# Kernel optimization log

Hardware: AMD Instinct MI355X
Metric: run time of the kernel (lower is better)

Reference implementation:

```python
import jax, jax.numpy as jnp
import numpy as np

B, N, C, H = 2, 2048, 512, 8
D = C // H  # head dim = 64
SCALE = C ** -0.5  # module uses heads_channels**-0.5 (full inner dim, not per-head)


def setup_inputs() -> dict:
    key = jax.random.key(0)
    ks = jax.random.split(key, 9)
    return {
        "q": jax.random.normal(ks[0], (B, N, C), jnp.float32),
        "kv": jax.random.normal(ks[1], (B, N, C), jnp.float32),
        "pos_q": jax.random.normal(ks[2], (B, N, D), jnp.float32),
        "pos_k": jax.random.normal(ks[3], (B, N, D), jnp.float32),
        "Wq": jax.random.normal(ks[4], (C, C), jnp.float32) * (C ** -0.5),
        "Wk": jax.random.normal(ks[5], (C, C), jnp.float32) * (C ** -0.5),
        "Wv": jax.random.normal(ks[6], (C, C), jnp.float32) * (C ** -0.5),
        "Wo": jax.random.normal(ks[7], (C, C), jnp.float32) * (C ** -0.5),
        "bo": jnp.zeros((C,), jnp.float32),
    }


def reference(q, kv, pos_q, pos_k, Wq, Wk, Wv, Wo, bo):
    # projections: [b n c] @ [c c] -> [b n c]
    qp = q @ Wq
    kp = kv @ Wk
    vp = kv @ Wv
    # split heads: b n (h d) -> b h n d
    split = lambda t: t.reshape(B, N, H, D).transpose(0, 2, 1, 3)
    qh, kh, vh = split(qp), split(kp), split(vp)
    # additive positional bias, broadcast over heads: b n d -> b 1 n d
    qh = qh + pos_q[:, None, :, :]
    kh = kh + pos_k[:, None, :, :]
    sim = jnp.einsum("bhid,bhjd->bhij", qh, kh) * SCALE
    attn = jax.nn.softmax(sim, axis=-1)
    out = jnp.einsum("bhij,bhjd->bhid", attn, vh)
    # merge heads: b h n d -> b n (h d)
    out = out.transpose(0, 2, 1, 3).reshape(B, N, C)
    return out @ Wo + bo
```

## Files before the change

### kernel.cpp

```cpp
#include <hip/hip_runtime.h>
#include <hip/hip_bf16.h>
#include <stdint.h>
#include <math.h>

static constexpr int kB = 2, kN = 2048, kC = 512, kH = 8, kD = 64;
static constexpr float kScaleL2E =
    (float)(0.044194173824159216 * 1.4426950408889634);
static constexpr int kSplit = 2;
static constexpr size_t kSegF = (size_t)kB * kN * kC;

typedef short bf16x8 __attribute__((ext_vector_type(8)));
typedef short bf16x4 __attribute__((ext_vector_type(4)));
typedef float f32x4  __attribute__((ext_vector_type(4)));

__device__ __forceinline__ float bf2f(unsigned short u) {
  union { unsigned int i; float f; } v; v.i = ((unsigned int)u) << 16; return v.f;
}
__device__ __forceinline__ unsigned short f2bf(float f) {
  union { float f; unsigned int i; } v; v.f = f;
  unsigned int x = v.i;
  return (unsigned short)((x + 0x7FFFu + ((x >> 16) & 1u)) >> 16);
}
__device__ __forceinline__ short f2bs(float f) { return (short)f2bf(f); }
__device__ __forceinline__ unsigned int pack2_t(float lo, float hi) {
  union { float f; unsigned int i; } a, b; a.f = lo; b.f = hi;
  return (b.i & 0xFFFF0000u) | (a.i >> 16);
}
__device__ __forceinline__ float fast_exp2(float x) {
#if __has_builtin(__builtin_amdgcn_exp2f)
  return __builtin_amdgcn_exp2f(x);
#else
  return exp2f(x);
#endif
}

__device__ __forceinline__ int vcol(int k) {
  return 32 * (k >> 5) + ((k >> 2) & 3) * 8 + ((k >> 4) & 1) * 4;
}

__global__ __launch_bounds__(256) void prep_kernel(
    const float* __restrict__ q, const float* __restrict__ kv,
    const float* __restrict__ Wq, const float* __restrict__ Wk,
    const float* __restrict__ Wv,
    unsigned short* __restrict__ qbf, unsigned short* __restrict__ kvbf,
    unsigned short* __restrict__ wT)
{
  const int t = threadIdx.x;
  if (blockIdx.z == 0) {
    const int gid = blockIdx.x * 256 + t;
    #pragma unroll
    for (int it = 0; it < 8; ++it) {
      int i4 = gid + it * 65536;
      float4 a = *(const float4*)(q + (size_t)i4 * 4);
      float4 b = *(const float4*)(kv + (size_t)i4 * 4);
      bf16x4 ab = {f2bs(a.x), f2bs(a.y), f2bs(a.z), f2bs(a.w)};
      bf16x4 bb = {f2bs(b.x), f2bs(b.y), f2bs(b.z), f2bs(b.w)};
      *(bf16x4*)(qbf + (size_t)i4 * 4) = ab;
      *(bf16x4*)(kvbf + (size_t)i4 * 4) = bb;
    }
  } else {
    if (blockIdx.x >= 192) return;
    const int wsel = blockIdx.x >> 6;
    const int tile = blockIdx.x & 63;
    const int tr = tile >> 3, tc = tile & 7;
    const float* W = (wsel == 0) ? Wq : (wsel == 1 ? Wk : Wv);
    unsigned short* out = wT + (size_t)wsel * kC * kC;

    __shared__ __align__(16) float Ts[64][68];
    #pragma unroll
    for (int it = 0; it < 4; ++it) {
      int e = t + it * 256;
      int r = e >> 4, c4 = (e & 15) * 4;
      *(float4*)&Ts[r][c4] =
          *(const float4*)(W + (size_t)(tr * 64 + r) * kC + tc * 64 + c4);
    }
    __syncthreads();
    const int n = t >> 2, ks = (t & 3) * 16;
    unsigned short* orow = out + (size_t)(tc * 64 + n) * kC + tr * 64 + ks;
    #pragma unroll
    for (int c = 0; c < 4; ++c) {
      ushort4 o;
      o.x = f2bf(Ts[ks + c * 4 + 0][n]);
      o.y = f2bf(Ts[ks + c * 4 + 1][n]);
      o.z = f2bf(Ts[ks + c * 4 + 2][n]);
      o.w = f2bf(Ts[ks + c * 4 + 3][n]);
      *(ushort4*)(orow + c * 4) = o;
    }
  }
}

__global__ __launch_bounds__(256) void proj_kernel(
    const unsigned short* __restrict__ qbf,
    const unsigned short* __restrict__ kvbf,
    const unsigned short* __restrict__ wT,
    const float* __restrict__ pos_q,
    const float* __restrict__ pos_k,
    unsigned short* __restrict__ qh,
    unsigned short* __restrict__ kh,
    unsigned short* __restrict__ vhT)
{
  const bool kvmode = (blockIdx.z == 1);
  const unsigned short* A = kvmode ? kvbf : qbf;
  const unsigned short* Bt0 = wT + (kvmode ? (size_t)kC * kC : 0);
  const unsigned short* Bt1 = wT + 2 * (size_t)kC * kC;

  __shared__ __align__(16) unsigned short As[2][128][72];
  __shared__ __align__(16) unsigned short Bs[2][2][64][72];

  const int t = threadIdx.x;
  const int w = t >> 6, lane = t & 63;
  const int l15 = lane & 15, quad = lane >> 4;
  const int m0 = blockIdx.x * 128;
  const int n0 = blockIdx.y * 64;

  const int sr = t >> 3, sc = (t & 7) * 8;

  bf16x8 pa[4], pb0[2], pb1[2];
  #pragma unroll
  for (int i = 0; i < 4; ++i)
    pa[i] = *(const bf16x8*)(A + (size_t)(m0 + sr + i * 32) * kC + sc);
  #pragma unroll
  for (int i = 0; i < 2; ++i)
    pb0[i] = *(const bf16x8*)(Bt0 + (size_t)(n0 + sr + i * 32) * kC + sc);
  if (kvmode)
    #pragma unroll
    for (int i = 0; i < 2; ++i)
      pb1[i] = *(const bf16x8*)(Bt1 + (size_t)(n0 + sr + i * 32) * kC + sc);

  #pragma unroll
  for (int i = 0; i < 4; ++i) *(bf16x8*)&As[0][sr + i * 32][sc] = pa[i];
  #pragma unroll
  for (int i = 0; i < 2; ++i) *(bf16x8*)&Bs[0][0][sr + i * 32][sc] = pb0[i];
  if (kvmode)
    #pragma unroll
    for (int i = 0; i < 2; ++i) *(bf16x8*)&Bs[0][1][sr + i * 32][sc] = pb1[i];

  #pragma unroll
  for (int i = 0; i < 4; ++i)
    pa[i] = *(const bf16x8*)(A + (size_t)(m0 + sr + i * 32) * kC + 64 + sc);
  #pragma unroll
  for (int i = 0; i < 2; ++i)
    pb0[i] = *(const bf16x8*)(Bt0 + (size_t)(n0 + sr + i * 32) * kC + 64 + sc);
  if (kvmode)
    #pragma unroll
    for (int i = 0; i < 2; ++i)
      pb1[i] = *(const bf16x8*)(Bt1 + (size_t)(n0 + sr + i * 32) * kC + 64 + sc);

  f32x4 acc0[2][4], acc1[2][4];
  #pragma unroll
  for (int si = 0; si < 2; ++si)
    #pragma unroll
    for (int ct = 0; ct < 4; ++ct) {
      acc0[si][ct] = (f32x4){0.f, 0.f, 0.f, 0.f};
      acc1[si][ct] = (f32x4){0.f, 0.f, 0.f, 0.f};
    }

  const int nkt = kC / 64;
  for (int it = 0; it < nkt; ++it) {
    __syncthreads();
    if (it + 1 < nkt) {
      const int wb = (it + 1) & 1;
      #pragma unroll
      for (int i = 0; i < 4; ++i) *(bf16x8*)&As[wb][sr + i * 32][sc] = pa[i];
      #pragma unroll
      for (int i = 0; i < 2; ++i) *(bf16x8*)&Bs[wb][0][sr + i * 32][sc] = pb0[i];
      if (kvmode)
        #pragma unroll
        for (int i = 0; i < 2; ++i) *(bf16x8*)&Bs[wb][1][sr + i * 32][sc] = pb1[i];
      if (it + 2 < nkt) {
        const int kn = (it + 2) * 64;
        #pragma unroll
        for (int i = 0; i < 4; ++i)
          pa[i] = *(const bf16x8*)(A + (size_t)(m0 + sr + i * 32) * kC + kn + sc);
        #pragma unroll
        for (int i = 0; i < 2; ++i)
          pb0[i] = *(const bf16x8*)(Bt0 + (size_t)(n0 + sr + i * 32) * kC + kn + sc);
        if (kvmode)
          #pragma unroll
          for (int i = 0; i < 2; ++i)
            pb1[i] = *(const bf16x8*)(Bt1 + (size_t)(n0 + sr + i * 32) * kC + kn + sc);
      }
    }
    const int ib = it & 1;
    bf16x8 a0[2], a1[2];
    #pragma unroll
    for (int si = 0; si < 2; ++si) {
      a0[si] = *(const bf16x8*)&As[ib][w * 32 + si * 16 + l15][quad * 8];
      a1[si] = *(const bf16x8*)&As[ib][w * 32 + si * 16 + l15][32 + quad * 8];
    }
    #pragma unroll
    for (int ct = 0; ct < 4; ++ct) {
      bf16x8 b0 = *(const bf16x8*)&Bs[ib][0][ct * 16 + l15][quad * 8];
      bf16x8 b1 = *(const bf16x8*)&Bs[ib][0][ct * 16 + l15][32 + quad * 8];
      #pragma unroll
      for (int si = 0; si < 2; ++si) {
        acc0[si][ct] = __builtin_amdgcn_mfma_f32_16x16x32_bf16(a0[si], b0, acc0[si][ct], 0, 0, 0);
        acc0[si][ct] = __builtin_amdgcn_mfma_f32_16x16x32_bf16(a1[si], b1, acc0[si][ct], 0, 0, 0);
      }
      if (kvmode) {
        bf16x8 c0 = *(const bf16x8*)&Bs[ib][1][ct * 16 + l15][quad * 8];
        bf16x8 c1 = *(const bf16x8*)&Bs[ib][1][ct * 16 + l15][32 + quad * 8];
        #pragma unroll
        for (int si = 0; si < 2; ++si) {
          acc1[si][ct] = __builtin_amdgcn_mfma_f32_16x16x32_bf16(a0[si], c0, acc1[si][ct], 0, 0, 0);
          acc1[si][ct] = __builtin_amdgcn_mfma_f32_16x16x32_bf16(a1[si], c1, acc1[si][ct], 0, 0, 0);
        }
      }
    }
  }

  const int h = n0 >> 6;
  if (!kvmode) {
    #pragma unroll
    for (int si = 0; si < 2; ++si)
      #pragma unroll
      for (int r = 0; r < 4; ++r) {
        int m = m0 + w * 32 + si * 16 + quad * 4 + r;
        int b = m >> 11, n_seq = m & (kN - 1);
        #pragma unroll
        for (int ct = 0; ct < 4; ++ct) {
          int d = ct * 16 + l15;
          float val = (acc0[si][ct][r] +
                       pos_q[((size_t)b * kN + n_seq) * kD + d]) * kScaleL2E;
          qh[(((size_t)b * kH + h) * kN + n_seq) * kD + d] = f2bf(val);
        }
      }
  } else {
    #pragma unroll
    for (int si = 0; si < 2; ++si)
      #pragma unroll
      for (int r = 0; r < 4; ++r) {
        int m = m0 + w * 32 + si * 16 + quad * 4 + r;
        int b = m >> 11, n_seq = m & (kN - 1);
        #pragma unroll
        for (int ct = 0; ct < 4; ++ct) {
          int d = ct * 16 + l15;
          float vk = acc0[si][ct][r] + pos_k[((size_t)b * kN + n_seq) * kD + d];
          kh[(((size_t)b * kH + h) * kN + n_seq) * kD + d] = f2bf(vk);
        }
      }
    __syncthreads();
    unsigned short (*Tv)[136] = (unsigned short(*)[136])&As[0][0][0];
    #pragma unroll
    for (int si = 0; si < 2; ++si)
      #pragma unroll
      for (int ct = 0; ct < 4; ++ct) {
        const int d = ct * 16 + l15;
        const int nl = w * 32 + si * 16 + quad * 4;
        unsigned int lo = (unsigned int)f2bf(acc1[si][ct][0]) |
                          ((unsigned int)f2bf(acc1[si][ct][1]) << 16);
        unsigned int hi = (unsigned int)f2bf(acc1[si][ct][2]) |
                          ((unsigned int)f2bf(acc1[si][ct][3]) << 16);
        *(unsigned int*)&Tv[d][nl]     = lo;
        *(unsigned int*)&Tv[d][nl + 2] = hi;
      }
    __syncthreads();
    const int c16 = t & 15, dr = t >> 4;
    const int b2 = m0 >> 11, nbase = m0 & (kN - 1);
    #pragma unroll
    for (int rep = 0; rep < 4; ++rep) {
      const int d = rep * 16 + dr;
      bf16x8 vv = *(const bf16x8*)&Tv[d][c16 * 8];
      *(bf16x8*)(vhT + (((size_t)(b2 * kH + h)) * kD + d) * kN + nbase + c16 * 8) = vv;
    }
  }
}

__global__ __launch_bounds__(256, 8) void attn_kernel(
    const unsigned short* __restrict__ qh,
    const unsigned short* __restrict__ kh,
    const unsigned short* __restrict__ vhT,
    unsigned short* __restrict__ opart,
    float* __restrict__ lbuf)
{
  const int sid = (blockIdx.x & 7) * 128 + (blockIdx.x >> 3);
  const int s  = sid >> 9;
  const int bh = (sid >> 5) & 15;
  const int q0 = (sid & 31) * 64;
  const int b = bh >> 3, h = bh & 7;
  const int kbase = s * (kN / kSplit);
  const int nkt = kN / kSplit / 64;
  const int t = threadIdx.x;
  const int w = t >> 6, lane = t & 63;
  const int l15 = lane & 15, quad = lane >> 4;

  __shared__ __align__(16) unsigned short Kb_s[2][64][72];
  __shared__ __align__(16) unsigned short Vt_s[2][64][72];

  const unsigned short* Qb = qh  + (size_t)bh * kN * kD;
  const unsigned short* Kb = kh  + (size_t)bh * kN * kD;
  const unsigned short* Vb = vhT + (size_t)bh * kD * kN;

  bf16x8 aq0, aq1;
  {
    const unsigned short* qrow = Qb + (size_t)(q0 + w * 16 + l15) * kD;
    aq0 = *(const bf16x8*)(qrow + quad * 8);
    aq1 = *(const bf16x8*)(qrow + 32 + quad * 8);
  }

  const int sr = t >> 3, sc = (t & 7) * 8, sr2 = sr + 32;
  const int vc1 = vcol(sc), vc2 = vcol(sc + 4);

  const unsigned short* pK0 = Kb + (size_t)(kbase + sr) * kD + sc;
  const unsigned short* pK1 = Kb + (size_t)(kbase + sr2) * kD + sc;
  const unsigned short* pV0 = Vb + (size_t)sr * kN + kbase + sc;
  const unsigned short* pV1 = Vb + (size_t)sr2 * kN + kbase + sc;
  const size_t kStepK = (size_t)64 * kD;

  {
    bf16x8 k0v = *(const bf16x8*)pK0;
    bf16x8 k1v = *(const bf16x8*)pK1;
    bf16x8 v0v = *(const bf16x8*)pV0;
    bf16x8 v1v = *(const bf16x8*)pV1;
    *(bf16x8*)&Kb_s[0][sr][sc]  = k0v;
    *(bf16x8*)&Kb_s[0][sr2][sc] = k1v;
    bf16x4 lo0 = {v0v[0], v0v[1], v0v[2], v0v[3]};
    bf16x4 hi0 = {v0v[4], v0v[5], v0v[6], v0v[7]};
    bf16x4 lo1 = {v1v[0], v1v[1], v1v[2], v1v[3]};
    bf16x4 hi1 = {v1v[4], v1v[5], v1v[6], v1v[7]};
    *(bf16x4*)&Vt_s[0][sr][vc1]  = lo0;
    *(bf16x4*)&Vt_s[0][sr][vc2]  = hi0;
    *(bf16x4*)&Vt_s[0][sr2][vc1] = lo1;
    *(bf16x4*)&Vt_s[0][sr2][vc2] = hi1;
  }
  pK0 += kStepK; pK1 += kStepK; pV0 += 64; pV1 += 64;
  bf16x8 pk0 = *(const bf16x8*)pK0;
  bf16x8 pk1 = *(const bf16x8*)pK1;
  bf16x8 pv0 = *(const bf16x8*)pV0;
  bf16x8 pv1 = *(const bf16x8*)pV1;

  f32x4 o[4];
  #pragma unroll
  for (int nt = 0; nt < 4; ++nt) o[nt] = (f32x4){0.f, 0.f, 0.f, 0.f};
  float l_run = 0.f;

  for (int i = 0; i < nkt; ++i) {
    __syncthreads();
    const unsigned short (*Kr)[72] = Kb_s[i & 1];
    const unsigned short (*Vr)[72] = Vt_s[i & 1];

    f32x4 sacc[4];
    __builtin_amdgcn_s_setprio(1);
    #pragma unroll
    for (int ct = 0; ct < 4; ++ct) {
      bf16x8 ak0 = *(const bf16x8*)&Kr[ct * 16 + l15][quad * 8];
      bf16x8 ak1 = *(const bf16x8*)&Kr[ct * 16 + l15][32 + quad * 8];
      f32x4 zz = (f32x4){0.f, 0.f, 0.f, 0.f};
      zz = __builtin_amdgcn_mfma_f32_16x16x32_bf16(ak0, aq0, zz, 0, 0, 0);
      zz = __builtin_amdgcn_mfma_f32_16x16x32_bf16(ak1, aq1, zz, 0, 0, 0);
      sacc[ct] = zz;
    }
    __builtin_amdgcn_s_setprio(0);

    union PB8 { unsigned int u[4]; bf16x8 v; } pb01, pb23;
    {
      float psum = 0.f;
      #pragma unroll
      for (int ct = 0; ct < 4; ++ct)
        #pragma unroll
        for (int r = 0; r < 4; ++r) {
          float p = fast_exp2(sacc[ct][r]);
          sacc[ct][r] = p;
          psum += p;
        }
      l_run += psum;
      pb01.u[0] = pack2_t(sacc[0][0], sacc[0][1]);
      pb01.u[1] = pack2_t(sacc[0][2], sacc[0][3]);
      pb01.u[2] = pack2_t(sacc[1][0], sacc[1][1]);
      pb01.u[3] = pack2_t(sacc[1][2], sacc[1][3]);
      pb23.u[0] = pack2_t(sacc[2][0], sacc[2][1]);
      pb23.u[1] = pack2_t(sacc[2][2], sacc[2][3]);
      pb23.u[2] = pack2_t(sacc[3][0], sacc[3][1]);
      pb23.u[3] = pack2_t(sacc[3][2], sacc[3][3]);
    }

    __builtin_amdgcn_s_setprio(1);
    #pragma unroll
    for (int nt = 0; nt < 4; ++nt) {
      bf16x8 av0 = *(const bf16x8*)&Vr[nt * 16 + l15][quad * 8];
      bf16x8 av1 = *(const bf16x8*)&Vr[nt * 16 + l15][32 + quad * 8];
      o[nt] = __builtin_amdgcn_mfma_f32_16x16x32_bf16(av0, pb01.v, o[nt], 0, 0, 0);
      o[nt] = __builtin_amdgcn_mfma_f32_16x16x32_bf16(av1, pb23.v, o[nt], 0, 0, 0);
    }
    __builtin_amdgcn_s_setprio(0);

    if (i + 1 < nkt) {
      unsigned short (*Kw)[72] = Kb_s[(i + 1) & 1];
      unsigned short (*Vw)[72] = Vt_s[(i + 1) & 1];
      *(bf16x8*)&Kw[sr][sc]  = pk0;
      *(bf16x8*)&Kw[sr2][sc] = pk1;
      bf16x4 lo0 = {pv0[0], pv0[1], pv0[2], pv0[3]};
      bf16x4 hi0 = {pv0[4], pv0[5], pv0[6], pv0[7]};
      bf16x4 lo1 = {pv1[0], pv1[1], pv1[2], pv1[3]};
      bf16x4 hi1 = {pv1[4], pv1[5], pv1[6], pv1[7]};
      *(bf16x4*)&Vw[sr][vc1]  = lo0;
      *(bf16x4*)&Vw[sr][vc2]  = hi0;
      *(bf16x4*)&Vw[sr2][vc1] = lo1;
      *(bf16x4*)&Vw[sr2][vc2] = hi1;
      if (i + 2 < nkt) {
        pK0 += kStepK; pK1 += kStepK; pV0 += 64; pV1 += 64;
        pk0 = *(const bf16x8*)pK0;
        pk1 = *(const bf16x8*)pK1;
        pv0 = *(const bf16x8*)pV0;
        pv1 = *(const bf16x8*)pV1;
      }
    }
  }

  l_run += __shfl_xor(l_run, 16);
  l_run += __shfl_xor(l_run, 32);
  if (quad == 0)
    lbuf[(size_t)(s * 16 + bh) * kN + q0 + w * 16 + l15] = l_run;

  __syncthreads();
  unsigned short (*Ot)[72] = (unsigned short(*)[72])&Kb_s[0][0][0];
  {
    const int ql = w * 16 + l15;
    #pragma unroll
    for (int nt = 0; nt < 4; ++nt) {
      unsigned int lo = (unsigned int)f2bf(o[nt][0]) |
                        ((unsigned int)f2bf(o[nt][1]) << 16);
      unsigned int hi = (unsigned int)f2bf(o[nt][2]) |
                        ((unsigned int)f2bf(o[nt][3]) << 16);
      const int d0 = nt * 16 + quad * 4;
      *(unsigned int*)&Ot[ql][d0]     = lo;
      *(unsigned int*)&Ot[ql][d0 + 2] = hi;
    }
  }
  __syncthreads();
  {
    unsigned short* od = opart + (size_t)s * kSegF;
    const int c8 = t & 7, qb = t >> 3;
    #pragma unroll
    for (int rep = 0; rep < 2; ++rep) {
      const int ql = rep * 32 + qb;
      bf16x8 vv = *(const bf16x8*)&Ot[ql][c8 * 8];
      *(bf16x8*)(od + ((size_t)b * kN + (q0 + ql)) * kC + h * kD + c8 * 8) = vv;
    }
  }
}

__global__ __launch_bounds__(256) void proj_out_kernel(
    const unsigned short* __restrict__ opart,
    const float* __restrict__ lbuf,
    const float* __restrict__ Wo,
    const float* __restrict__ bo,
    float* __restrict__ out)
{
  __shared__ __align__(16) unsigned short Wt[2][64][72];

  const int t = threadIdx.x;
  const int w = t >> 6, lane = t & 63;
  const int l15 = lane & 15, quad = lane >> 4;
  const int m0 = blockIdx.x * 64;
  const int n0 = blockIdx.y * 64;

  const int m = m0 + w * 16 + l15;
  const int nseq = m & (kN - 1);
  const int bb = m >> 11;
  const size_t arow = (size_t)m * kC;

  ushort4 pw[4];
  #pragma unroll
  for (int i = 0; i < 4; ++i) {
    int e = t + i * 256;
    int r = e >> 4, c4 = (e & 15) * 4;
    float4 wv = *(const float4*)(Wo + (size_t)r * kC + n0 + c4);
    pw[i] = make_ushort4(f2bf(wv.x), f2bf(wv.y), f2bf(wv.z), f2bf(wv.w));
  }
  #pragma unroll
  for (int i = 0; i < 4; ++i) {
    int e = t + i * 256;
    int r = e >> 4, c4 = (e & 15) * 4;
    Wt[0][c4 + 0][r] = pw[i].x;
    Wt[0][c4 + 1][r] = pw[i].y;
    Wt[0][c4 + 2][r] = pw[i].z;
    Wt[0][c4 + 3][r] = pw[i].w;
  }
  #pragma unroll
  for (int i = 0; i < 4; ++i) {
    int e = t + i * 256;
    int r = e >> 4, c4 = (e & 15) * 4;
    float4 wv = *(const float4*)(Wo + (size_t)(64 + r) * kC + n0 + c4);
    pw[i] = make_ushort4(f2bf(wv.x), f2bf(wv.y), f2bf(wv.z), f2bf(wv.w));
  }

  f32x4 acc[4];
  #pragma unroll
  for (int ct = 0; ct < 4; ++ct) acc[ct] = (f32x4){0.f, 0.f, 0.f, 0.f};

  const int nkt = kC / 64;
  for (int it = 0; it < nkt; ++it) {
    const int k0 = it * 64;
    __syncthreads();
    if (it + 1 < nkt) {
      const int wb = (it + 1) & 1;
      #pragma unroll
      for (int i = 0; i < 4; ++i) {
        int e = t + i * 256;
        int r = e >> 4, c4 = (e & 15) * 4;
        Wt[wb][c4 + 0][r] = pw[i].x;
        Wt[wb][c4 + 1][r] = pw[i].y;
        Wt[wb][c4 + 2][r] = pw[i].z;
        Wt[wb][c4 + 3][r] = pw[i].w;
      }
      if (it + 2 < nkt) {
        const int kn = (it + 2) * 64;
        #pragma unroll
        for (int i = 0; i < 4; ++i) {
          int e = t + i * 256;
          int r = e >> 4, c4 = (e & 15) * 4;
          float4 wv = *(const float4*)(Wo + (size_t)(kn + r) * kC + n0 + c4);
          pw[i] = make_ushort4(f2bf(wv.x), f2bf(wv.y), f2bf(wv.z), f2bf(wv.w));
        }
      }
    }

    const int h = k0 >> 6;
    const int bh = bb * 8 + h;
    float lsum = 0.f;
    #pragma unroll
    for (int s = 0; s < kSplit; ++s)
      lsum += lbuf[(size_t)(s * 16 + bh) * kN + nseq];
    const float wgt = 1.f / lsum;

    float af0[8] = {}, af1[8] = {};
    #pragma unroll
    for (int s = 0; s < kSplit; ++s) {
      bf16x8 v0 = *(const bf16x8*)(opart + (size_t)s * kSegF + arow + k0 + quad * 8);
      bf16x8 v1 = *(const bf16x8*)(opart + (size_t)s * kSegF + arow + k0 + 32 + quad * 8);
      #pragma unroll
      for (int j = 0; j < 8; ++j) {
        af0[j] += bf2f((unsigned short)v0[j]);
        af1[j] += bf2f((unsigned short)v1[j]);
      }
    }
    bf16x8 a0, a1;
    #pragma unroll
    for (int j = 0; j < 8; ++j) {
      a0[j] = (short)f2bf(af0[j] * wgt);
      a1[j] = (short)f2bf(af1[j] * wgt);
    }

    const int ib = it & 1;
    #pragma unroll
    for (int ct = 0; ct < 4; ++ct) {
      bf16x8 b0 = *(const bf16x8*)&Wt[ib][ct * 16 + l15][quad * 8];
      bf16x8 b1 = *(const bf16x8*)&Wt[ib][ct * 16 + l15][32 + quad * 8];
      acc[ct] = __builtin_amdgcn_mfma_f32_16x16x32_bf16(a0, b0, acc[ct], 0, 0, 0);
      acc[ct] = __builtin_amdgcn_mfma_f32_16x16x32_bf16(a1, b1, acc[ct], 0, 0, 0);
    }
  }

  #pragma unroll
  for (int ct = 0; ct < 4; ++ct) {
    int n = n0 + ct * 16 + l15;
    float bb2 = bo[n];
    #pragma unroll
    for (int r = 0; r < 4; ++r) {
      int mm = m0 + w * 16 + quad * 4 + r;
      out[(size_t)mm * kC + n] = acc[ct][r] + bb2;
    }
  }
}

extern "C" void kernel_launch(void* const* d_in, const int* in_sizes, int n_in,
                              void* d_out, int out_size, void* d_ws, size_t ws_size,
                              hipStream_t stream) {
  (void)in_sizes; (void)n_in; (void)out_size; (void)ws_size;
  const float* q     = (const float*)d_in[0];
  const float* kv    = (const float*)d_in[1];
  const float* pos_q = (const float*)d_in[2];
  const float* pos_k = (const float*)d_in[3];
  const float* Wq    = (const float*)d_in[4];
  const float* Wk    = (const float*)d_in[5];
  const float* Wv    = (const float*)d_in[6];
  const float* Wo    = (const float*)d_in[7];
  const float* bo    = (const float*)d_in[8];
  float* out = (float*)d_out;

  const size_t seg = (size_t)kB * kH * kN * kD;

  unsigned short* qbf  = (unsigned short*)d_ws;
  unsigned short* kvbf = qbf + seg;
  unsigned short* wT   = kvbf + seg;
  unsigned short* qhp  = wT + 3 * (size_t)kC * kC;
  unsigned short* khp  = qhp + seg;
  unsigned short* vtp  = khp + seg;
  unsigned short* opart = vtp + seg;
  float* lbuf = (float*)(opart + (size_t)kSplit * kSegF);

  dim3 blk(256);
  prep_kernel<<<dim3(256, 1, 2), blk, 0, stream>>>(q, kv, Wq, Wk, Wv, qbf, kvbf, wT);
  proj_kernel<<<dim3(32, 8, 2), blk, 0, stream>>>(qbf, kvbf, wT, pos_q, pos_k,
                                                  qhp, khp, vtp);
  attn_kernel<<<dim3(1024), blk, 0, stream>>>(qhp, khp, vtp, opart, lbuf);
  proj_out_kernel<<<dim3(64, 8), blk, 0, stream>>>(opart, lbuf, Wo, bo, out);
}
```

Before: 141.5 us.

## Load K/V MFMA operands directly from global memory, dropping LDS staging

The attention kernel no longer stages K and V tiles through double-buffered shared memory. Each wave now reads its MFMA operands straight from global memory (or L2), and the per-tile __syncthreads barriers go away. Shared memory is reduced to a single output staging tile, which may allow higher occupancy. The cost is that all four waves redundantly load the same K/V data, the V loads become narrower 8-byte reads, and the software prefetch that hid latency is gone.

```diff
diff --git a/kernel.cpp b/kernel.cpp
--- a/kernel.cpp
+++ b/kernel.cpp
@@ -32,10 +32,6 @@
 #else
   return exp2f(x);
 #endif
-}
-
-__device__ __forceinline__ int vcol(int k) {
-  return 32 * (k >> 5) + ((k >> 2) & 3) * 8 + ((k >> 4) & 1) * 4;
 }
 
 __global__ __launch_bounds__(256) void prep_kernel(
@@ -284,8 +280,7 @@
   const int w = t >> 6, lane = t & 63;
   const int l15 = lane & 15, quad = lane >> 4;
 
-  __shared__ __align__(16) unsigned short Kb_s[2][64][72];
-  __shared__ __align__(16) unsigned short Vt_s[2][64][72];
+  __shared__ __align__(16) unsigned short Ot[64][72];
 
   const unsigned short* Qb = qh  + (size_t)bh * kN * kD;
   const unsigned short* Kb = kh  + (size_t)bh * kN * kD;
@@ -298,36 +293,8 @@
     aq1 = *(const bf16x8*)(qrow + 32 + quad * 8);
   }
 
-  const int sr = t >> 3, sc = (t & 7) * 8, sr2 = sr + 32;
-  const int vc1 = vcol(sc), vc2 = vcol(sc + 4);
-
-  const unsigned short* pK0 = Kb + (size_t)(kbase + sr) * kD + sc;
-  const unsigned short* pK1 = Kb + (size_t)(kbase + sr2) * kD + sc;
-  const unsigned short* pV0 = Vb + (size_t)sr * kN + kbase + sc;
-  const unsigned short* pV1 = Vb + (size_t)sr2 * kN + kbase + sc;
-  const size_t kStepK = (size_t)64 * kD;
-
-  {
-    bf16x8 k0v = *(const bf16x8*)pK0;
-    bf16x8 k1v = *(const bf16x8*)pK1;
-    bf16x8 v0v = *(const bf16x8*)pV0;
-    bf16x8 v1v = *(const bf16x8*)pV1;
-    *(bf16x8*)&Kb_s[0][sr][sc]  = k0v;
-    *(bf16x8*)&Kb_s[0][sr2][sc] = k1v;
-    bf16x4 lo0 = {v0v[0], v0v[1], v0v[2], v0v[3]};
-    bf16x4 hi0 = {v0v[4], v0v[5], v0v[6], v0v[7]};
-    bf16x4 lo1 = {v1v[0], v1v[1], v1v[2], v1v[3]};
-    bf16x4 hi1 = {v1v[4], v1v[5], v1v[6], v1v[7]};
-    *(bf16x4*)&Vt_s[0][sr][vc1]  = lo0;
-    *(bf16x4*)&Vt_s[0][sr][vc2]  = hi0;
-    *(bf16x4*)&Vt_s[0][sr2][vc1] = lo1;
-    *(bf16x4*)&Vt_s[0][sr2][vc2] = hi1;
-  }
-  pK0 += kStepK; pK1 += kStepK; pV0 += 64; pV1 += 64;
-  bf16x8 pk0 = *(const bf16x8*)pK0;
-  bf16x8 pk1 = *(const bf16x8*)pK1;
-  bf16x8 pv0 = *(const bf16x8*)pV0;
-  bf16x8 pv1 = *(const bf16x8*)pV1;
+  const unsigned short* Kl = Kb + (size_t)(kbase + l15) * kD + quad * 8;
+  const unsigned short* Vl = Vb + (size_t)l15 * kN + kbase + quad * 4;
 
   f32x4 o[4];
   #pragma unroll
@@ -335,16 +302,16 @@
   float l_run = 0.f;
 
   for (int i = 0; i < nkt; ++i) {
-    __syncthreads();
-    const unsigned short (*Kr)[72] = Kb_s[i & 1];
-    const unsigned short (*Vr)[72] = Vt_s[i & 1];
+    const unsigned short* Kt = Kl + (size_t)(i * 64) * kD;
+    const unsigned short* Vt = Vl + i * 64;
 
     f32x4 sacc[4];
     __builtin_amdgcn_s_setprio(1);
     #pragma unroll
     for (int ct = 0; ct < 4; ++ct) {
-      bf16x8 ak0 = *(const bf16x8*)&Kr[ct * 16 + l15][quad * 8];
-      bf16x8 ak1 = *(const bf16x8*)&Kr[ct * 16 + l15][32 + quad * 8];
+      const unsigned short* kr = Kt + (size_t)(ct * 16) * kD;
+      bf16x8 ak0 = *(const bf16x8*)kr;
+      bf16x8 ak1 = *(const bf16x8*)(kr + 32);
       f32x4 zz = (f32x4){0.f, 0.f, 0.f, 0.f};
       zz = __builtin_amdgcn_mfma_f32_16x16x32_bf16(ak0, aq0, zz, 0, 0, 0);
       zz = __builtin_amdgcn_mfma_f32_16x16x32_bf16(ak1, aq1, zz, 0, 0, 0);
@@ -377,34 +344,16 @@
     __builtin_amdgcn_s_setprio(1);
     #pragma unroll
     for (int nt = 0; nt < 4; ++nt) {
-      bf16x8 av0 = *(const bf16x8*)&Vr[nt * 16 + l15][quad * 8];
-      bf16x8 av1 = *(const bf16x8*)&Vr[nt * 16 + l15][32 + quad * 8];
-      o[nt] = __builtin_amdgcn_mfma_f32_16x16x32_bf16(av0, pb01.v, o[nt], 0, 0, 0);
-      o[nt] = __builtin_amdgcn_mfma_f32_16x16x32_bf16(av1, pb23.v, o[nt], 0, 0, 0);
+      const unsigned short* vr = Vt + (size_t)(nt * 16) * kN;
+      union AV { bf16x4 h[2]; bf16x8 v; } av0, av1;
+      av0.h[0] = *(const bf16x4*)vr;
+      av0.h[1] = *(const bf16x4*)(vr + 16);
+      av1.h[0] = *(const bf16x4*)(vr + 32);
+      av1.h[1] = *(const bf16x4*)(vr + 48);
+      o[nt] = __builtin_amdgcn_mfma_f32_16x16x32_bf16(av0.v, pb01.v, o[nt], 0, 0, 0);
+      o[nt] = __builtin_amdgcn_mfma_f32_16x16x32_bf16(av1.v, pb23.v, o[nt], 0, 0, 0);
     }
     __builtin_amdgcn_s_setprio(0);
-
-    if (i + 1 < nkt) {
-      unsigned short (*Kw)[72] = Kb_s[(i + 1) & 1];
-      unsigned short (*Vw)[72] = Vt_s[(i + 1) & 1];
-      *(bf16x8*)&Kw[sr][sc]  = pk0;
-      *(bf16x8*)&Kw[sr2][sc] = pk1;
-      bf16x4 lo0 = {pv0[0], pv0[1], pv0[2], pv0[3]};
-      bf16x4 hi0 = {pv0[4], pv0[5], pv0[6], pv0[7]};
-      bf16x4 lo1 = {pv1[0], pv1[1], pv1[2], pv1[3]};
-      bf16x4 hi1 = {pv1[4], pv1[5], pv1[6], pv1[7]};
-      *(bf16x4*)&Vw[sr][vc1]  = lo0;
-      *(bf16x4*)&Vw[sr][vc2]  = hi0;
-      *(bf16x4*)&Vw[sr2][vc1] = lo1;
-      *(bf16x4*)&Vw[sr2][vc2] = hi1;
-      if (i + 2 < nkt) {
-        pK0 += kStepK; pK1 += kStepK; pV0 += 64; pV1 += 64;
-        pk0 = *(const bf16x8*)pK0;
-        pk1 = *(const bf16x8*)pK1;
-        pv0 = *(const bf16x8*)pV0;
-        pv1 = *(const bf16x8*)pV1;
-      }
-    }
   }
 
   l_run += __shfl_xor(l_run, 16);
@@ -412,8 +361,6 @@
   if (quad == 0)
     lbuf[(size_t)(s * 16 + bh) * kN + q0 + w * 16 + l15] = l_run;
 
-  __syncthreads();
-  unsigned short (*Ot)[72] = (unsigned short(*)[72])&Kb_s[0][0][0];
   {
     const int ql = w * 16 + l15;
     #pragma unroll
```

After: 283.3 us. 100% more time.
